# Kernel tuning notes

Measured on AMD Instinct MI355X. Metric: run time of the kernel, lower is better.

## Reference

```python
import jax, jax.numpy as jnp
import numpy as np

N_NODES = 100000
N_EDGES = 1600000
DIM = 128
N_LAYERS = 3
N_GRAPHS = 512
BN_EPS = 1e-5


def setup_inputs() -> dict:
    key = jax.random.key(0)
    ks = jax.random.split(key, 8)
    x = jax.random.normal(ks[0], (N_NODES, DIM), dtype=jnp.float32)
    edge_index = jax.random.randint(ks[1], (2, N_EDGES), 0, N_NODES)
    batch = jnp.sort(jax.random.randint(ks[2], (N_NODES,), 0, N_GRAPHS))
    s = 1.0 / np.sqrt(DIM).astype(np.float32)
    # GIN MLP per layer: Linear(DIM->DIM), ReLU, Linear(DIM->DIM); stacked over layers
    W1 = jax.random.normal(ks[3], (N_LAYERS, DIM, DIM), dtype=jnp.float32) * s
    b1 = jnp.zeros((N_LAYERS, DIM), jnp.float32)
    W2 = jax.random.normal(ks[4], (N_LAYERS, DIM, DIM), dtype=jnp.float32) * s
    b2 = jnp.zeros((N_LAYERS, DIM), jnp.float32)
    # BatchNorm1d affine params
    gamma = jnp.ones((N_LAYERS, DIM), jnp.float32)
    beta = jnp.zeros((N_LAYERS, DIM), jnp.float32)
    return dict(x=x, edge_index=edge_index, batch=batch,
                W1=W1, b1=b1, W2=W2, b2=b2, gamma=gamma, beta=beta)


def reference(x, edge_index, batch, W1, b1, W2, b2, gamma, beta):
    src, dst = edge_index[0], edge_index[1]
    n = x.shape[0]
    z = x
    zs = []
    for l in range(N_LAYERS):
        # GINConv (eps=0): h_i = MLP((1+eps)*z_i + sum_{j in N(i)} z_j)
        agg = jax.ops.segment_sum(z[src], dst, num_segments=n)  # scatter-add messages
        h = agg + z
        h = jnp.maximum(h @ W1[l] + b1[l], 0.0) @ W2[l] + b2[l]
        h = jnp.maximum(h, 0.0)  # F.relu
        # BatchNorm1d (training-mode batch statistics, biased variance)
        mu = h.mean(axis=0)
        var = h.var(axis=0)
        z = (h - mu) * jax.lax.rsqrt(var + BN_EPS) * gamma[l] + beta[l]
        zs.append(z)
    gs = [jax.ops.segment_sum(zl, batch, num_segments=N_GRAPHS) for zl in zs]
    z_out = jnp.concatenate(zs, axis=1)   # [N, L*DIM]
    g_out = jnp.concatenate(gs, axis=1)   # [G, L*DIM]
    return (z_out, g_out)
```

## Files before the change

### kernel.cpp

```cpp
#include <hip/hip_runtime.h>

#define N_NODES 100000
#define N_EDGES 1600000
#define DIM 128
#define NLAYERS 3
#define NGRAPHS 512
#define BN_EPS 1e-5f

#define SCHUNK 512
#define SBLOCKS ((N_NODES + SCHUNK - 1) / SCHUNK)

#define WPL 5120
#define WCH 10240
#define LSTRIDE 81920

typedef __attribute__((ext_vector_type(8))) short short8;
typedef __attribute__((ext_vector_type(4))) float f32x4;

__device__ __forceinline__ unsigned f2b(float f) {
  unsigned u = __float_as_uint(f);
  return (u + 0x7FFFu + ((u >> 16) & 1u)) >> 16;
}
__device__ __forceinline__ float b2f(unsigned hw) {
  return __uint_as_float(hw << 16);
}

__global__ __launch_bounds__(256) void hist_kernel(const int* __restrict__ dst,
                                                   int* __restrict__ deg) {
  for (int e = blockIdx.x * blockDim.x + threadIdx.x; e < N_EDGES;
       e += gridDim.x * blockDim.x)
    atomicAdd(&deg[dst[e]], 1);
}

__global__ __launch_bounds__(256) void partial_kernel(const int* __restrict__ deg,
                                                      int* __restrict__ bsum) {
  __shared__ int red[256];
  const int t = threadIdx.x;
  const int i0 = blockIdx.x * SCHUNK + 2 * t;
  int s = 0;
  if (i0 + 1 < N_NODES) {
    const int2 v = *(const int2*)(deg + i0);
    s = v.x + v.y;
  } else if (i0 < N_NODES) {
    s = deg[i0];
  }
  red[t] = s;
  __syncthreads();
  for (int off = 128; off > 0; off >>= 1) {
    if (t < off) red[t] += red[t + off];
    __syncthreads();
  }
  if (t == 0) bsum[blockIdx.x] = red[0];
}

__global__ __launch_bounds__(256) void bscan_kernel(const int* __restrict__ bsum,
                                                    int* __restrict__ boff,
                                                    int* __restrict__ row_ptr) {
  __shared__ int s[256];
  const int t = threadIdx.x;
  const int v = (t < SBLOCKS) ? bsum[t] : 0;
  s[t] = v;
  __syncthreads();
  for (int off = 1; off < 256; off <<= 1) {
    int u = (t >= off) ? s[t - off] : 0;
    __syncthreads();
    s[t] += u;
    __syncthreads();
  }
  if (t < SBLOCKS) boff[t] = s[t] - v;
  if (t == SBLOCKS - 1) row_ptr[N_NODES] = s[t];
}

__global__ __launch_bounds__(256) void emit_kernel(const int* __restrict__ deg,
                                                   const int* __restrict__ boff,
                                                   int* __restrict__ row_ptr,
                                                   int* __restrict__ cursor) {
  __shared__ int s[256];
  const int t = threadIdx.x;
  const int i0 = blockIdx.x * SCHUNK + 2 * t;
  int d0 = 0, d1 = 0;
  if (i0 + 1 < N_NODES) {
    const int2 v = *(const int2*)(deg + i0);
    d0 = v.x; d1 = v.y;
  } else if (i0 < N_NODES) {
    d0 = deg[i0];
  }
  const int pair = d0 + d1;
  s[t] = pair;
  __syncthreads();
  for (int off = 1; off < 256; off <<= 1) {
    int u = (t >= off) ? s[t - off] : 0;
    __syncthreads();
    s[t] += u;
    __syncthreads();
  }
  const int base = boff[blockIdx.x] + s[t] - pair;
  if (i0 + 1 < N_NODES) {
    const int2 rp = make_int2(base, base + d0);
    *(int2*)(row_ptr + i0) = rp;
    *(int2*)(cursor + i0) = rp;
  } else if (i0 < N_NODES) {
    row_ptr[i0] = base;
    cursor[i0] = base;
  }
}

__global__ __launch_bounds__(256) void fill_kernel(const int* __restrict__ src,
                                                   const int* __restrict__ dst,
                                                   int* __restrict__ cursor,
                                                   int* __restrict__ col) {
  for (int e = blockIdx.x * blockDim.x + threadIdx.x; e < N_EDGES;
       e += gridDim.x * blockDim.x) {
    const int d = dst[e];
    const int pos = atomicAdd(&cursor[d], 1);
    col[pos] = src[e];
  }
}

__global__ __launch_bounds__(256) void wcvt_kernel(const float* __restrict__ W1,
                                                   const float* __restrict__ W2,
                                                   ushort* __restrict__ wsplit) {
  const int id = blockIdx.x * 256 + threadIdx.x;
  const int n = id & 127;
  const int kk = (id >> 7) & 31;
  const int kc = (id >> 12) & 3;
  const int p = (id >> 14) & 1;
  const int l = id >> 15;
  const float* src = p ? W2 : W1;
  const float v = src[(size_t)l * 16384 + (kc * 32 + kk) * 128 + n];
  const unsigned hi = f2b(v);
  const unsigned lo = f2b(v - b2f(hi));
  ushort* dst = wsplit + (size_t)((l * 2 + p) * 4 + kc) * WCH + n * 40 + kk;
  dst[0] = (ushort)hi;
  dst[WPL] = (ushort)lo;
}

__global__ __launch_bounds__(256) void agg_kernel(const float* __restrict__ zin,
                                                  int zstride,
                                                  const int* __restrict__ row_ptr,
                                                  const int* __restrict__ col,
                                                  float* __restrict__ agg) {
  const int w = (blockIdx.x * 256 + threadIdx.x) >> 6;
  const int lane = threadIdx.x & 63;
  if (w >= N_NODES) return;
  const int start = row_ptr[w];
  const int end = row_ptr[w + 1];

  float2 acc = ((const float2*)(zin + (size_t)w * zstride))[lane];
  int j = start;
  for (; j + 8 <= end; j += 8) {
    const int c0 = col[j], c1 = col[j + 1], c2 = col[j + 2], c3 = col[j + 3];
    const int c4 = col[j + 4], c5 = col[j + 5], c6 = col[j + 6], c7 = col[j + 7];
    const float2 v0 = ((const float2*)(zin + (size_t)c0 * zstride))[lane];
    const float2 v1 = ((const float2*)(zin + (size_t)c1 * zstride))[lane];
    const float2 v2 = ((const float2*)(zin + (size_t)c2 * zstride))[lane];
    const float2 v3 = ((const float2*)(zin + (size_t)c3 * zstride))[lane];
    const float2 v4 = ((const float2*)(zin + (size_t)c4 * zstride))[lane];
    const float2 v5 = ((const float2*)(zin + (size_t)c5 * zstride))[lane];
    const float2 v6 = ((const float2*)(zin + (size_t)c6 * zstride))[lane];
    const float2 v7 = ((const float2*)(zin + (size_t)c7 * zstride))[lane];
    acc.x += ((v0.x + v1.x) + (v2.x + v3.x)) + ((v4.x + v5.x) + (v6.x + v7.x));
    acc.y += ((v0.y + v1.y) + (v2.y + v3.y)) + ((v4.y + v5.y) + (v6.y + v7.y));
  }
  for (; j + 4 <= end; j += 4) {
    const int c0 = col[j], c1 = col[j + 1], c2 = col[j + 2], c3 = col[j + 3];
    const float2 v0 = ((const float2*)(zin + (size_t)c0 * zstride))[lane];
    const float2 v1 = ((const float2*)(zin + (size_t)c1 * zstride))[lane];
    const float2 v2 = ((const float2*)(zin + (size_t)c2 * zstride))[lane];
    const float2 v3 = ((const float2*)(zin + (size_t)c3 * zstride))[lane];
    acc.x += (v0.x + v1.x) + (v2.x + v3.x);
    acc.y += (v0.y + v1.y) + (v2.y + v3.y);
  }
  for (; j < end; ++j) {
    const int c = col[j];
    const float2 v = ((const float2*)(zin + (size_t)c * zstride))[lane];
    acc.x += v.x;
    acc.y += v.y;
  }
  ((float2*)(agg + (size_t)w * DIM))[lane] = acc;
}

__global__ __launch_bounds__(256) void mlp_kernel(
    const float* __restrict__ X,
    const ushort* __restrict__ Wsp,
    const float* __restrict__ b1,
    const float* __restrict__ b2,
    float* __restrict__ out,
    int lcol,
    float* __restrict__ bnsum) {
  __shared__ __align__(16) ushort smem[2 * 64 * 136 + WCH];
  ushort* Xh = smem;
  ushort* Xl = smem + 64 * 136;
  ushort* Wc = smem + 2 * 64 * 136;
  float* red = (float*)smem;

  const int tid = threadIdx.x;
  const int l = tid & 63, wv = tid >> 6;
  const int lr = l & 15, lg = l >> 4;
  const int n0 = blockIdx.x * 64;

  for (int i = tid; i < 64 * 32; i += 256) {
    const int row = i >> 5, c4 = (i & 31) * 4;
    float4 v = make_float4(0.f, 0.f, 0.f, 0.f);
    if (n0 + row < N_NODES) v = *(const float4*)(X + (size_t)(n0 + row) * 128 + c4);
    ushort4 hi, lo;
    hi.x = (ushort)f2b(v.x); lo.x = (ushort)f2b(v.x - b2f(hi.x));
    hi.y = (ushort)f2b(v.y); lo.y = (ushort)f2b(v.y - b2f(hi.y));
    hi.z = (ushort)f2b(v.z); lo.z = (ushort)f2b(v.z - b2f(hi.z));
    hi.w = (ushort)f2b(v.w); lo.w = (ushort)f2b(v.w - b2f(hi.w));
    *(ushort4*)(Xh + row * 136 + c4) = hi;
    *(ushort4*)(Xl + row * 136 + c4) = lo;
  }

  f32x4 acc[8];
#pragma unroll
  for (int p = 0; p < 2; ++p) {
#pragma unroll
    for (int nt = 0; nt < 8; ++nt) acc[nt] = {0.f, 0.f, 0.f, 0.f};
#pragma unroll
    for (int kc = 0; kc < 4; ++kc) {
      __syncthreads();
      {
        const uint4* wsrc = (const uint4*)(Wsp + (size_t)(p * 4 + kc) * WCH);
        for (int i = tid; i < WCH / 8; i += 256) ((uint4*)Wc)[i] = wsrc[i];
      }
      __syncthreads();
      const short8 ah = *(const short8*)(Xh + (wv * 16 + lr) * 136 + kc * 32 + lg * 8);
      const short8 al = *(const short8*)(Xl + (wv * 16 + lr) * 136 + kc * 32 + lg * 8);
#pragma unroll
      for (int nt = 0; nt < 8; ++nt) {
        const short8 bh = *(const short8*)(Wc + (nt * 16 + lr) * 40 + lg * 8);
        const short8 bl = *(const short8*)(Wc + WPL + (nt * 16 + lr) * 40 + lg * 8);
        acc[nt] = __builtin_amdgcn_mfma_f32_16x16x32_bf16(ah, bh, acc[nt], 0, 0, 0);
        acc[nt] = __builtin_amdgcn_mfma_f32_16x16x32_bf16(al, bh, acc[nt], 0, 0, 0);
        acc[nt] = __builtin_amdgcn_mfma_f32_16x16x32_bf16(ah, bl, acc[nt], 0, 0, 0);
      }
    }
    if (p == 0) {
      __syncthreads();
      float b1v[8];
#pragma unroll
      for (int nt = 0; nt < 8; ++nt) b1v[nt] = b1[nt * 16 + lr];
#pragma unroll
      for (int nt = 0; nt < 8; ++nt) {
#pragma unroll
        for (int r = 0; r < 4; ++r) {
          const float h = fmaxf(acc[nt][r] + b1v[nt], 0.f);
          const unsigned hi = f2b(h);
          const unsigned lo = f2b(h - b2f(hi));
          Xh[(wv * 16 + lg * 4 + r) * 136 + nt * 16 + lr] = (ushort)hi;
          Xl[(wv * 16 + lg * 4 + r) * 136 + nt * 16 + lr] = (ushort)lo;
        }
      }
    }
  }

  float s[8], q2[8];
  {
    float b2v[8];
#pragma unroll
    for (int nt = 0; nt < 8; ++nt) b2v[nt] = b2[nt * 16 + lr];
#pragma unroll
    for (int nt = 0; nt < 8; ++nt) { s[nt] = 0.f; q2[nt] = 0.f; }
#pragma unroll
    for (int nt = 0; nt < 8; ++nt) {
#pragma unroll
      for (int r = 0; r < 4; ++r) {
        const int n = n0 + wv * 16 + lg * 4 + r;
        const float h = fmaxf(acc[nt][r] + b2v[nt], 0.f);
        if (n < N_NODES) {
          out[(size_t)n * (NLAYERS * DIM) + lcol + nt * 16 + lr] = h;
          s[nt] += h;
          q2[nt] += h * h;
        }
      }
    }
  }
  __syncthreads();

  const int rg = tid >> 4, cb = tid & 15;
#pragma unroll
  for (int nt = 0; nt < 8; ++nt) red[rg * 128 + nt * 16 + cb] = s[nt];
  __syncthreads();
  if (tid < 128) {
    float t = 0.f;
#pragma unroll
    for (int g = 0; g < 16; ++g) t += red[g * 128 + tid];
    unsafeAtomicAdd(&bnsum[tid], t);
  }
  __syncthreads();
#pragma unroll
  for (int nt = 0; nt < 8; ++nt) red[rg * 128 + nt * 16 + cb] = q2[nt];
  __syncthreads();
  if (tid < 128) {
    float t = 0.f;
#pragma unroll
    for (int g = 0; g < 16; ++g) t += red[g * 128 + tid];
    unsafeAtomicAdd(&bnsum[128 + tid], t);
  }
}

__global__ __launch_bounds__(128) void bn_finalize_kernel(
    const float* __restrict__ bnsum, const float* __restrict__ gamma,
    const float* __restrict__ beta, float* __restrict__ bnfin) {
  const int c = threadIdx.x;
  const float inv_n = 1.f / (float)N_NODES;
  const float mu = bnsum[c] * inv_n;
  const float var = bnsum[128 + c] * inv_n - mu * mu;
  const float inv = rsqrtf(var + BN_EPS);
  const float sc = gamma[c] * inv;
  bnfin[c] = sc;
  bnfin[128 + c] = beta[c] - mu * sc;
}

__global__ __launch_bounds__(256) void bn_norm_kernel(float* __restrict__ zcol,
                                                      const float* __restrict__ bnfin) {
  const int idx = blockIdx.x * 256 + threadIdx.x;
  if (idx >= N_NODES * 32) return;
  const int n = idx >> 5, c4 = idx & 31;
  const float4 sc = ((const float4*)bnfin)[c4];
  const float4 sh = ((const float4*)(bnfin + 128))[c4];
  float4* p = (float4*)(zcol + (size_t)n * (NLAYERS * DIM)) + c4;
  float4 v = *p;
  v.x = fmaf(v.x, sc.x, sh.x);
  v.y = fmaf(v.y, sc.y, sh.y);
  v.z = fmaf(v.z, sc.z, sh.z);
  v.w = fmaf(v.w, sc.w, sh.w);
  *p = v;
}

__global__ __launch_bounds__(128) void pool_kernel(const float* __restrict__ zout,
                                                   const int* __restrict__ batch,
                                                   float* __restrict__ gout) {
  const int g = blockIdx.x / 3;
  const int chunk = blockIdx.x % 3;
  const int c = chunk * 128 + threadIdx.x;
  int lo = 0, hi = N_NODES;
  while (lo < hi) {
    const int m = (lo + hi) >> 1;
    if (batch[m] < g) lo = m + 1; else hi = m;
  }
  int lo2 = lo, hi2 = N_NODES;
  while (lo2 < hi2) {
    const int m = (lo2 + hi2) >> 1;
    if (batch[m] < g + 1) lo2 = m + 1; else hi2 = m;
  }
  float acc = 0.f;
  for (int n = lo; n < lo2; ++n) acc += zout[(size_t)n * (NLAYERS * DIM) + c];
  gout[(size_t)g * (NLAYERS * DIM) + c] = acc;
}

extern "C" void kernel_launch(void* const* d_in, const int* in_sizes, int n_in,
                              void* d_out, int out_size, void* d_ws, size_t ws_size,
                              hipStream_t stream) {
  const float* x = (const float*)d_in[0];
  const int* ei = (const int*)d_in[1];
  const int* src = ei;
  const int* dst = ei + N_EDGES;
  const int* batch = (const int*)d_in[2];
  const float* W1 = (const float*)d_in[3];
  const float* b1 = (const float*)d_in[4];
  const float* W2 = (const float*)d_in[5];
  const float* b2 = (const float*)d_in[6];
  const float* gamma = (const float*)d_in[7];
  const float* beta = (const float*)d_in[8];
  float* out = (float*)d_out;
  float* gout = out + (size_t)N_NODES * NLAYERS * DIM;

  char* ws = (char*)d_ws;
  size_t off = 0;
  auto alloc = [&](size_t bytes) -> void* {
    off = (off + 511) & ~(size_t)511;
    void* p = ws + off;
    off += bytes;
    return p;
  };
  int* row_ptr = (int*)alloc((N_NODES + 1) * sizeof(int));
  int* cursor = (int*)alloc(N_NODES * sizeof(int));
  int* deg = (int*)alloc(N_NODES * sizeof(int));
  int* col = (int*)alloc(N_EDGES * sizeof(int));
  int* bsum = (int*)alloc(SBLOCKS * sizeof(int));
  int* boff = (int*)alloc(SBLOCKS * sizeof(int));
  float* agg = (float*)alloc((size_t)N_NODES * DIM * sizeof(float));
  ushort* wsplit = (ushort*)alloc((size_t)NLAYERS * LSTRIDE * sizeof(ushort));
  float* bnsum = (float*)alloc(NLAYERS * 256 * sizeof(float));
  float* bnfin = (float*)alloc(NLAYERS * 256 * sizeof(float));

  hipMemsetAsync(deg, 0, N_NODES * sizeof(int), stream);
  hipMemsetAsync(bnsum, 0, NLAYERS * 256 * sizeof(float), stream);

  hist_kernel<<<2048, 256, 0, stream>>>(dst, deg);
  partial_kernel<<<SBLOCKS, 256, 0, stream>>>(deg, bsum);
  bscan_kernel<<<1, 256, 0, stream>>>(bsum, boff, row_ptr);
  emit_kernel<<<SBLOCKS, 256, 0, stream>>>(deg, boff, row_ptr, cursor);
  fill_kernel<<<2048, 256, 0, stream>>>(src, dst, cursor, col);
  wcvt_kernel<<<384, 256, 0, stream>>>(W1, W2, wsplit);

  for (int l = 0; l < NLAYERS; ++l) {
    const float* zin = (l == 0) ? x : (out + (size_t)(l - 1) * DIM);
    const int zstride = (l == 0) ? DIM : NLAYERS * DIM;
    agg_kernel<<<(N_NODES * 64 + 255) / 256, 256, 0, stream>>>(zin, zstride,
                                                               row_ptr, col, agg);
    mlp_kernel<<<(N_NODES + 63) / 64, 256, 0, stream>>>(
        agg, wsplit + (size_t)l * LSTRIDE, b1 + (size_t)l * DIM,
        b2 + (size_t)l * DIM, out, l * DIM, bnsum + l * 256);
    bn_finalize_kernel<<<1, 128, 0, stream>>>(bnsum + l * 256, gamma + l * DIM,
                                              beta + l * DIM, bnfin + l * 256);
    bn_norm_kernel<<<(N_NODES * 32 + 255) / 256, 256, 0, stream>>>(
        out + (size_t)l * DIM, bnfin + l * 256);
  }
  pool_kernel<<<NGRAPHS * 3, 128, 0, stream>>>(out, batch, gout);
}
```

Before: 1.172 ms.

## Gather neighbor features in bf16 and emit pre-split hi/lo aggregates

Adds a bf16 copy of node features (from x initially, and written by the batchnorm kernel for later layers). The aggregation kernel gathers these half-width rows, accumulates in fp32, and writes bf16 hi/lo split aggregates. The MLP kernel then just copies the split rows instead of converting. This halves the random-gather bytes per edge but rounds neighbor features to bf16, which may loosen accuracy versus the fp32 reference.

```diff
diff --git a/kernel.cpp b/kernel.cpp
--- a/kernel.cpp
+++ b/kernel.cpp
@@ -115,6 +115,19 @@
     const int pos = atomicAdd(&cursor[d], 1);
     col[pos] = src[e];
   }
+}
+
+__global__ __launch_bounds__(256) void xcvt_kernel(const float* __restrict__ x,
+                                                   ushort* __restrict__ zb) {
+  const int i = blockIdx.x * 256 + threadIdx.x;
+  const float4 a = ((const float4*)x)[2 * i];
+  const float4 b = ((const float4*)x)[2 * i + 1];
+  uint4 o;
+  o.x = (f2b(a.y) << 16) | f2b(a.x);
+  o.y = (f2b(a.w) << 16) | f2b(a.z);
+  o.z = (f2b(b.y) << 16) | f2b(b.x);
+  o.w = (f2b(b.w) << 16) | f2b(b.z);
+  ((uint4*)zb)[i] = o;
 }
 
 __global__ __launch_bounds__(256) void wcvt_kernel(const float* __restrict__ W1,
@@ -135,53 +148,59 @@
   dst[WPL] = (ushort)lo;
 }
 
-__global__ __launch_bounds__(256) void agg_kernel(const float* __restrict__ zin,
-                                                  int zstride,
+__global__ __launch_bounds__(256) void agg_kernel(const ushort* __restrict__ zb,
                                                   const int* __restrict__ row_ptr,
                                                   const int* __restrict__ col,
-                                                  float* __restrict__ agg) {
+                                                  ushort* __restrict__ aggh,
+                                                  ushort* __restrict__ aggl) {
   const int w = (blockIdx.x * 256 + threadIdx.x) >> 6;
   const int lane = threadIdx.x & 63;
   if (w >= N_NODES) return;
   const int start = row_ptr[w];
   const int end = row_ptr[w + 1];
 
-  float2 acc = ((const float2*)(zin + (size_t)w * zstride))[lane];
+  const unsigned us = ((const unsigned*)(zb + (size_t)w * 128))[lane];
+  float ax = b2f(us & 0xFFFFu), ay = b2f(us >> 16);
   int j = start;
   for (; j + 8 <= end; j += 8) {
     const int c0 = col[j], c1 = col[j + 1], c2 = col[j + 2], c3 = col[j + 3];
     const int c4 = col[j + 4], c5 = col[j + 5], c6 = col[j + 6], c7 = col[j + 7];
-    const float2 v0 = ((const float2*)(zin + (size_t)c0 * zstride))[lane];
-    const float2 v1 = ((const float2*)(zin + (size_t)c1 * zstride))[lane];
-    const float2 v2 = ((const float2*)(zin + (size_t)c2 * zstride))[lane];
-    const float2 v3 = ((const float2*)(zin + (size_t)c3 * zstride))[lane];
-    const float2 v4 = ((const float2*)(zin + (size_t)c4 * zstride))[lane];
-    const float2 v5 = ((const float2*)(zin + (size_t)c5 * zstride))[lane];
-    const float2 v6 = ((const float2*)(zin + (size_t)c6 * zstride))[lane];
-    const float2 v7 = ((const float2*)(zin + (size_t)c7 * zstride))[lane];
-    acc.x += ((v0.x + v1.x) + (v2.x + v3.x)) + ((v4.x + v5.x) + (v6.x + v7.x));
-    acc.y += ((v0.y + v1.y) + (v2.y + v3.y)) + ((v4.y + v5.y) + (v6.y + v7.y));
+    const unsigned u0 = ((const unsigned*)(zb + (size_t)c0 * 128))[lane];
+    const unsigned u1 = ((const unsigned*)(zb + (size_t)c1 * 128))[lane];
+    const unsigned u2 = ((const unsigned*)(zb + (size_t)c2 * 128))[lane];
+    const unsigned u3 = ((const unsigned*)(zb + (size_t)c3 * 128))[lane];
+    const unsigned u4 = ((const unsigned*)(zb + (size_t)c4 * 128))[lane];
+    const unsigned u5 = ((const unsigned*)(zb + (size_t)c5 * 128))[lane];
+    const unsigned u6 = ((const unsigned*)(zb + (size_t)c6 * 128))[lane];
+    const unsigned u7 = ((const unsigned*)(zb + (size_t)c7 * 128))[lane];
+    ax += ((b2f(u0 & 0xFFFFu) + b2f(u1 & 0xFFFFu)) + (b2f(u2 & 0xFFFFu) + b2f(u3 & 0xFFFFu))) +
+          ((b2f(u4 & 0xFFFFu) + b2f(u5 & 0xFFFFu)) + (b2f(u6 & 0xFFFFu) + b2f(u7 & 0xFFFFu)));
+    ay += ((b2f(u0 >> 16) + b2f(u1 >> 16)) + (b2f(u2 >> 16) + b2f(u3 >> 16))) +
+          ((b2f(u4 >> 16) + b2f(u5 >> 16)) + (b2f(u6 >> 16) + b2f(u7 >> 16)));
   }
   for (; j + 4 <= end; j += 4) {
     const int c0 = col[j], c1 = col[j + 1], c2 = col[j + 2], c3 = col[j + 3];
-    const float2 v0 = ((const float2*)(zin + (size_t)c0 * zstride))[lane];
-    const float2 v1 = ((const float2*)(zin + (size_t)c1 * zstride))[lane];
-    const float2 v2 = ((const float2*)(zin + (size_t)c2 * zstride))[lane];
-    const float2 v3 = ((const float2*)(zin + (size_t)c3 * zstride))[lane];
-    acc.x += (v0.x + v1.x) + (v2.x + v3.x);
-    acc.y += (v0.y + v1.y) + (v2.y + v3.y);
+    const unsigned u0 = ((const unsigned*)(zb + (size_t)c0 * 128))[lane];
+    const unsigned u1 = ((const unsigned*)(zb + (size_t)c1 * 128))[lane];
+    const unsigned u2 = ((const unsigned*)(zb + (size_t)c2 * 128))[lane];
+    const unsigned u3 = ((const unsigned*)(zb + (size_t)c3 * 128))[lane];
+    ax += (b2f(u0 & 0xFFFFu) + b2f(u1 & 0xFFFFu)) + (b2f(u2 & 0xFFFFu) + b2f(u3 & 0xFFFFu));
+    ay += (b2f(u0 >> 16) + b2f(u1 >> 16)) + (b2f(u2 >> 16) + b2f(u3 >> 16));
   }
   for (; j < end; ++j) {
-    const int c = col[j];
-    const float2 v = ((const float2*)(zin + (size_t)c * zstride))[lane];
-    acc.x += v.x;
-    acc.y += v.y;
-  }
-  ((float2*)(agg + (size_t)w * DIM))[lane] = acc;
+    const unsigned uc = ((const unsigned*)(zb + (size_t)col[j] * 128))[lane];
+    ax += b2f(uc & 0xFFFFu);
+    ay += b2f(uc >> 16);
+  }
+  const unsigned hx = f2b(ax), hy = f2b(ay);
+  const unsigned lx = f2b(ax - b2f(hx)), ly = f2b(ay - b2f(hy));
+  ((unsigned*)(aggh + (size_t)w * 128))[lane] = (hy << 16) | hx;
+  ((unsigned*)(aggl + (size_t)w * 128))[lane] = (ly << 16) | lx;
 }
 
 __global__ __launch_bounds__(256) void mlp_kernel(
-    const float* __restrict__ X,
+    const ushort* __restrict__ Xhp,
+    const ushort* __restrict__ Xlp,
     const ushort* __restrict__ Wsp,
     const float* __restrict__ b1,
     const float* __restrict__ b2,
@@ -199,17 +218,15 @@
   const int lr = l & 15, lg = l >> 4;
   const int n0 = blockIdx.x * 64;
 
-  for (int i = tid; i < 64 * 32; i += 256) {
-    const int row = i >> 5, c4 = (i & 31) * 4;
-    float4 v = make_float4(0.f, 0.f, 0.f, 0.f);
-    if (n0 + row < N_NODES) v = *(const float4*)(X + (size_t)(n0 + row) * 128 + c4);
-    ushort4 hi, lo;
-    hi.x = (ushort)f2b(v.x); lo.x = (ushort)f2b(v.x - b2f(hi.x));
-    hi.y = (ushort)f2b(v.y); lo.y = (ushort)f2b(v.y - b2f(hi.y));
-    hi.z = (ushort)f2b(v.z); lo.z = (ushort)f2b(v.z - b2f(hi.z));
-    hi.w = (ushort)f2b(v.w); lo.w = (ushort)f2b(v.w - b2f(hi.w));
-    *(ushort4*)(Xh + row * 136 + c4) = hi;
-    *(ushort4*)(Xl + row * 136 + c4) = lo;
+  for (int i = tid; i < 64 * 16; i += 256) {
+    const int row = i >> 4, ch = i & 15;
+    int4 vh = make_int4(0, 0, 0, 0), vl = vh;
+    if (n0 + row < N_NODES) {
+      vh = *(const int4*)(Xhp + (size_t)(n0 + row) * 128 + ch * 8);
+      vl = *(const int4*)(Xlp + (size_t)(n0 + row) * 128 + ch * 8);
+    }
+    *(int4*)(Xh + row * 136 + ch * 8) = vh;
+    *(int4*)(Xl + row * 136 + ch * 8) = vl;
   }
 
   f32x4 acc[8];
@@ -314,7 +331,8 @@
 }
 
 __global__ __launch_bounds__(256) void bn_norm_kernel(float* __restrict__ zcol,
-                                                      const float* __restrict__ bnfin) {
+                                                      const float* __restrict__ bnfin,
+                                                      ushort* __restrict__ zb) {
   const int idx = blockIdx.x * 256 + threadIdx.x;
   if (idx >= N_NODES * 32) return;
   const int n = idx >> 5, c4 = idx & 31;
@@ -327,6 +345,12 @@
   v.z = fmaf(v.z, sc.z, sh.z);
   v.w = fmaf(v.w, sc.w, sh.w);
   *p = v;
+  if (zb) {
+    uint2 o;
+    o.x = (f2b(v.y) << 16) | f2b(v.x);
+    o.y = (f2b(v.w) << 16) | f2b(v.z);
+    *(uint2*)(zb + (size_t)n * 128 + c4 * 4) = o;
+  }
 }
 
 __global__ __launch_bounds__(128) void pool_kernel(const float* __restrict__ zout,
@@ -381,7 +405,9 @@
   int* col = (int*)alloc(N_EDGES * sizeof(int));
   int* bsum = (int*)alloc(SBLOCKS * sizeof(int));
   int* boff = (int*)alloc(SBLOCKS * sizeof(int));
-  float* agg = (float*)alloc((size_t)N_NODES * DIM * sizeof(float));
+  ushort* zb = (ushort*)alloc((size_t)N_NODES * 128 * sizeof(ushort));
+  ushort* aggh = (ushort*)alloc((size_t)N_NODES * 128 * sizeof(ushort));
+  ushort* aggl = (ushort*)alloc((size_t)N_NODES * 128 * sizeof(ushort));
   ushort* wsplit = (ushort*)alloc((size_t)NLAYERS * LSTRIDE * sizeof(ushort));
   float* bnsum = (float*)alloc(NLAYERS * 256 * sizeof(float));
   float* bnfin = (float*)alloc(NLAYERS * 256 * sizeof(float));
@@ -394,20 +420,19 @@
   bscan_kernel<<<1, 256, 0, stream>>>(bsum, boff, row_ptr);
   emit_kernel<<<SBLOCKS, 256, 0, stream>>>(deg, boff, row_ptr, cursor);
   fill_kernel<<<2048, 256, 0, stream>>>(src, dst, cursor, col);
+  xcvt_kernel<<<(N_NODES * DIM / 8) / 256, 256, 0, stream>>>(x, zb);
   wcvt_kernel<<<384, 256, 0, stream>>>(W1, W2, wsplit);
 
   for (int l = 0; l < NLAYERS; ++l) {
-    const float* zin = (l == 0) ? x : (out + (size_t)(l - 1) * DIM);
-    const int zstride = (l == 0) ? DIM : NLAYERS * DIM;
-    agg_kernel<<<(N_NODES * 64 + 255) / 256, 256, 0, stream>>>(zin, zstride,
-                                                               row_ptr, col, agg);
+    agg_kernel<<<(N_NODES * 64 + 255) / 256, 256, 0, stream>>>(zb, row_ptr, col,
+                                                               aggh, aggl);
     mlp_kernel<<<(N_NODES + 63) / 64, 256, 0, stream>>>(
-        agg, wsplit + (size_t)l * LSTRIDE, b1 + (size_t)l * DIM,
+        aggh, aggl, wsplit + (size_t)l * LSTRIDE, b1 + (size_t)l * DIM,
         b2 + (size_t)l * DIM, out, l * DIM, bnsum + l * 256);
     bn_finalize_kernel<<<1, 128, 0, stream>>>(bnsum + l * 256, gamma + l * DIM,
                                               beta + l * DIM, bnfin + l * 256);
     bn_norm_kernel<<<(N_NODES * 32 + 255) / 256, 256, 0, stream>>>(
-        out + (size_t)l * DIM, bnfin + l * 256);
+        out + (size_t)l * DIM, bnfin + l * 256, (l < NLAYERS - 1) ? zb : nullptr);
   }
   pool_kernel<<<NGRAPHS * 3, 128, 0, stream>>>(out, batch, gout);
 }
```

Measured after the change: 1.026 ms. -12.5%, faster.
